# Optimization experiments

Hardware: AMD Instinct MI355X
Metric: run time of the kernel (lower is better)

The kernel has to match this reference:

```python
import jax, jax.numpy as jnp
import numpy as np

EMBED_DIM = 1024
KEY_SIZE = 1024
VALUE_SIZE = 1024


def setup_inputs() -> dict:
    key = jax.random.key(0)
    k1, k2, k3, k4, k5 = jax.random.split(key, 5)
    B, L = 4, 4096
    s = 1.0 / np.sqrt(EMBED_DIM)
    return {
        "x": jax.random.normal(k1, (B, L, EMBED_DIM), dtype=jnp.float32),
        # torch nn.Linear weights: [out_features, in_features]
        "Wq": jax.random.normal(k2, (KEY_SIZE, EMBED_DIM), dtype=jnp.float32) * s,
        "Wk": jax.random.normal(k3, (KEY_SIZE, EMBED_DIM), dtype=jnp.float32) * s,
        "Wv": jax.random.normal(k4, (VALUE_SIZE, EMBED_DIM), dtype=jnp.float32) * s,
        "Wo": jax.random.normal(k5, (EMBED_DIM, VALUE_SIZE), dtype=jnp.float32) * s,
    }


def reference(x, Wq, Wk, Wv, Wo):
    # x: [B, L, E]
    q = jnp.einsum("ble,ke->blk", x, Wq)  # [B, L, K]
    k = jnp.einsum("ble,ke->blk", x, Wk)  # [B, L, K]
    v = jnp.einsum("ble,ve->blv", x, Wv)  # [B, L, V]
    K = k.shape[-1]
    # transposed (feature-axial) attention: att over feature dims, contracting seq L
    att = jnp.einsum("blk,blj->bkj", q, k) / jnp.sqrt(jnp.asarray(K, x.dtype))  # [B, K, K]
    att = jax.nn.softmax(att, axis=-1)
    # out[b,l,k] = sum_j att[b,k,j] * v[b,l,j]  (matmul(att, v^T) then transpose)
    out = jnp.einsum("bkj,blj->blk", att, v)  # [B, L, K]
    return jnp.einsum("blv,ev->ble", out, Wo)  # [B, L, E]
```

## Files before the change

### kernel.cpp

```cpp
#include <hip/hip_runtime.h>
#include <hip/hip_bf16.h>

typedef unsigned short u16;
typedef __bf16 bf16x8 __attribute__((ext_vector_type(8)));
typedef float f32x4 __attribute__((ext_vector_type(4)));
typedef unsigned short ushort8 __attribute__((ext_vector_type(8)));

#define AS1 __attribute__((address_space(1)))
#define AS3 __attribute__((address_space(3)))

__device__ inline u16 f2bf(float f) {
  union { float f; unsigned int u; } c; c.f = f;
  unsigned int u = c.u;
  return (u16)((u + 0x7fffu + ((u >> 16) & 1u)) >> 16);
}
__device__ inline float bf2f(u16 v) {
  union { unsigned int u; float f; } c; c.u = ((unsigned int)v) << 16;
  return c.f;
}

__global__ __launch_bounds__(256) void cvt_x_dual(const float* __restrict__ x,
                                                  u16* __restrict__ xbf,
                                                  u16* __restrict__ xT) {
  __shared__ u16 tile[64][68];
  const int t = threadIdx.x;
  const long e0 = (long)blockIdx.x * 64;
  const long l0 = (long)blockIdx.y * 64;
  const long b  = blockIdx.z;
  const int tr = t >> 4, tc = t & 15;
#pragma unroll
  for (int i = 0; i < 4; ++i) {
    const int r = tr + i * 16;
    const long gl = b * 4096 + l0 + r;
    float4 v = *reinterpret_cast<const float4*>(x + gl * 1024 + e0 + tc * 4);
    ushort4 o;
    o.x = f2bf(v.x); o.y = f2bf(v.y); o.z = f2bf(v.z); o.w = f2bf(v.w);
    *reinterpret_cast<ushort4*>(xbf + gl * 1024 + e0 + tc * 4) = o;
    *reinterpret_cast<ushort4*>(&tile[r][tc * 4]) = o;
  }
  __syncthreads();
#pragma unroll
  for (int i = 0; i < 4; ++i) {
    const int c = tr + i * 16;
    ushort4 o;
    o.x = tile[tc * 4 + 0][c]; o.y = tile[tc * 4 + 1][c];
    o.z = tile[tc * 4 + 2][c]; o.w = tile[tc * 4 + 3][c];
    *reinterpret_cast<ushort4*>(xT + b * (1024L * 4096) + (e0 + c) * 4096 + l0 + tc * 4) = o;
  }
}

__global__ __launch_bounds__(256) void cvt_w4(const float* __restrict__ a, const float* __restrict__ b,
                                              const float* __restrict__ c, const float* __restrict__ d,
                                              u16* __restrict__ oa, u16* __restrict__ ob,
                                              u16* __restrict__ oc, u16* __restrict__ od) {
  int i = blockIdx.x * 256 + threadIdx.x;
  const int which = i >> 18;
  const int j = i & 262143;
  const float* src = which == 0 ? a : which == 1 ? b : which == 2 ? c : d;
  u16* dst = which == 0 ? oa : which == 1 ? ob : which == 2 ? oc : od;
  float4 v = reinterpret_cast<const float4*>(src)[j];
  ushort4 o;
  o.x = f2bf(v.x); o.y = f2bf(v.y); o.z = f2bf(v.z); o.w = f2bf(v.w);
  reinterpret_cast<ushort4*>(dst)[j] = o;
}

__global__ __launch_bounds__(256) void transpose_bf16(
    const u16* __restrict__ src, long sLd, long sZ,
    u16* __restrict__ dst, long dLd, long dZ) {
  __shared__ u16 tile[64][68];
  const int t = threadIdx.x;
  const long r0 = (long)blockIdx.y * 64;
  const long c0 = (long)blockIdx.x * 64;
  const long z = blockIdx.z;
  const int tr = t >> 4, tc = t & 15;
#pragma unroll
  for (int i = 0; i < 4; ++i) {
    const int r = tr + i * 16;
    ushort4 v = *reinterpret_cast<const ushort4*>(src + z * sZ + (r0 + r) * sLd + c0 + tc * 4);
    *reinterpret_cast<ushort4*>(&tile[r][tc * 4]) = v;
  }
  __syncthreads();
#pragma unroll
  for (int i = 0; i < 4; ++i) {
    const int c = tr + i * 16;
    ushort4 o;
    o.x = tile[tc * 4 + 0][c]; o.y = tile[tc * 4 + 1][c];
    o.z = tile[tc * 4 + 2][c]; o.w = tile[tc * 4 + 3][c];
    *reinterpret_cast<ushort4*>(dst + z * dZ + (c0 + c) * dLd + r0 + tc * 4) = o;
  }
}

__device__ __forceinline__ void stage_half(const u16* __restrict__ g, long ld, int k0,
                                           u16* dst, int t) {
#pragma unroll
  for (int i = 0; i < 2; ++i) {
    const int c = i * 512 + t;
    const int r = c >> 3;
    const int s = c & 7;
    const int col = ((s ^ (r & 7)) << 3) + k0;
    __builtin_amdgcn_global_load_lds((const AS1 void*)(g + (long)r * ld + col),
                                     (AS3 void*)(dst + c * 8), 16, 0, 0);
  }
}

template<int N16>
__device__ __forceinline__ void stage_rows256(const u16* __restrict__ g, long ld, int k0,
                                              u16* dst, int t) {
#pragma unroll
  for (int i = 0; i < N16; ++i) {
    const int c = i * 256 + t;
    const int r = c >> 3;
    const int s = c & 7;
    const int col = ((s ^ (r & 7)) << 3) + k0;
    __builtin_amdgcn_global_load_lds((const AS1 void*)(g + (long)r * ld + col),
                                     (AS3 void*)(dst + c * 8), 16, 0, 0);
  }
}

__device__ __forceinline__ bf16x8 frag_ld(const u16* s, int row, int colb) {
  return *reinterpret_cast<const bf16x8*>(
      reinterpret_cast<const char*>(s) + row * 128 + (colb ^ ((row & 7) << 4)));
}

#define XCD_DECODE2(TM, TN)                                                  \
  const int nxy = gridDim.x * gridDim.y;                                     \
  int flat = blockIdx.x + gridDim.x * blockIdx.y + nxy * blockIdx.z;         \
  const int total = nxy * gridDim.z;                                         \
  const int qq = total >> 3;                                                 \
  flat = (flat & 7) * qq + (flat >> 3);                                      \
  const int z = flat / nxy;                                                  \
  const int wg = flat % nxy;                                                 \
  const long m0 = (long)(wg % gridDim.x) * (TM);                             \
  const long n0 = (long)(wg / gridDim.x) * (TN);

#define BAR_PRE()       do { asm volatile("s_waitcnt vmcnt(6)" ::: "memory"); \
                             __builtin_amdgcn_s_barrier(); \
                             asm volatile("" ::: "memory"); } while (0)
#define BAR_POST()      do { asm volatile("" ::: "memory"); \
                             __builtin_amdgcn_s_barrier(); \
                             asm volatile("" ::: "memory"); } while (0)

template<bool OUT_F32>
__global__ __launch_bounds__(512, 2) void gemm_nt256(
    const u16* __restrict__ A, long lda, long sAz4, long sAz1,
    const u16* __restrict__ B, long ldb, long sBz4, long sBz1,
    void* __restrict__ Cv, long ldc, long sCz4, long sCz1,
    long cBatch, int cShift,
    int K, float scale)
{
  __shared__ u16 sm[2 * 32768] __attribute__((aligned(16)));

  const int t = threadIdx.x;
  XCD_DECODE2(256, 256);
  const long azoff = (long)(z >> 2) * sAz4 + (long)(z & 3) * sAz1;
  const long bzoff = (long)(z >> 2) * sBz4 + (long)(z & 3) * sBz1;
  const u16* Ab = A + azoff + m0 * lda;
  const u16* Bb = B + bzoff + n0 * ldb;

  const int wid = t >> 6, lane = t & 63;
  const int lhi = lane >> 4, llo = lane & 15;
  const int wm = wid >> 2, wn = wid & 3;

  f32x4 acc[2][4][2][2] = {};
  const int NT = K >> 6;

  stage_half(Ab, lda, 0, sm, t);
  stage_half(Bb + 128 * ldb, ldb, 0, sm + 16384 + 8192, t);
  stage_half(Bb, ldb, 0, sm + 16384, t);
  stage_half(Ab + 128 * lda, lda, 0, sm + 8192, t);
  stage_half(Ab, lda, 64, sm + 32768, t);
  stage_half(Bb + 128 * ldb, ldb, 64, sm + 32768 + 16384 + 8192, t);
  asm volatile("s_waitcnt vmcnt(4)" ::: "memory");
  __builtin_amdgcn_s_barrier();
  asm volatile("" ::: "memory");

  for (int kt = 0; kt < NT; ++kt) {
    const int kb = kt & 1;
    u16* bc = sm + kb * 32768;
    u16* bn = sm + (kb ^ 1) * 32768;
    const u16* sAc = bc;
    const u16* sBc = bc + 16384;
    const int k1 = ((kt + 1 < NT) ? kt + 1 : 0) << 6;
    const int k2 = ((kt + 2 < NT) ? kt + 2 : kt + 2 - NT) << 6;

    bf16x8 a[4][2], bl[2][2], bh[2][2];

#pragma unroll
    for (int fr = 0; fr < 4; ++fr)
#pragma unroll
      for (int kk = 0; kk < 2; ++kk)
        a[fr][kk] = frag_ld(sAc, wm * 64 + fr * 16 + llo, (kk << 6) + (lhi << 4));
#pragma unroll
    for (int fc = 0; fc < 2; ++fc)
#pragma unroll
      for (int kk = 0; kk < 2; ++kk)
        bl[fc][kk] = frag_ld(sBc, wn * 32 + fc * 16 + llo, (kk << 6) + (lhi << 4));
    stage_half(Bb, ldb, k1, bn + 16384, t);
    BAR_PRE();
    __builtin_amdgcn_s_setprio(1);
#pragma unroll
    for (int fr = 0; fr < 4; ++fr)
#pragma unroll
      for (int fc = 0; fc < 2; ++fc)
#pragma unroll
        for (int kk = 0; kk < 2; ++kk)
          acc[0][fr][0][fc] = __builtin_amdgcn_mfma_f32_16x16x32_bf16(a[fr][kk], bl[fc][kk], acc[0][fr][0][fc], 0, 0, 0);
    __builtin_amdgcn_s_setprio(0);
    BAR_POST();

#pragma unroll
    for (int fc = 0; fc < 2; ++fc)
#pragma unroll
      for (int kk = 0; kk < 2; ++kk)
        bh[fc][kk] = frag_ld(sBc, 128 + wn * 32 + fc * 16 + llo, (kk << 6) + (lhi << 4));
    stage_half(Ab + 128 * lda, lda, k1, bn + 8192, t);
    BAR_PRE();
    __builtin_amdgcn_s_setprio(1);
#pragma unroll
    for (int fr = 0; fr < 4; ++fr)
#pragma unroll
      for (int fc = 0; fc < 2; ++fc)
#pragma unroll
        for (int kk = 0; kk < 2; ++kk)
          acc[0][fr][1][fc] = __builtin_amdgcn_mfma_f32_16x16x32_bf16(a[fr][kk], bh[fc][kk], acc[0][fr][1][fc], 0, 0, 0);
    __builtin_amdgcn_s_setprio(0);
    BAR_POST();

#pragma unroll
    for (int fr = 0; fr < 4; ++fr)
#pragma unroll
      for (int kk = 0; kk < 2; ++kk)
        a[fr][kk] = frag_ld(sAc, 128 + wm * 64 + fr * 16 + llo, (kk << 6) + (lhi << 4));
    stage_half(Ab, lda, k2, bc, t);
    BAR_PRE();
    __builtin_amdgcn_s_setprio(1);
#pragma unroll
    for (int fr = 0; fr < 4; ++fr)
#pragma unroll
      for (int fc = 0; fc < 2; ++fc)
#pragma unroll
        for (int kk = 0; kk < 2; ++kk)
          acc[1][fr][1][fc] = __builtin_amdgcn_mfma_f32_16x16x32_bf16(a[fr][kk], bh[fc][kk], acc[1][fr][1][fc], 0, 0, 0);
    __builtin_amdgcn_s_setprio(0);
    BAR_POST();

    stage_half(Bb + 128 * ldb, ldb, k2, bc + 16384 + 8192, t);
    BAR_PRE();
    __builtin_amdgcn_s_setprio(1);
#pragma unroll
    for (int fr = 0; fr < 4; ++fr)
#pragma unroll
      for (int fc = 0; fc < 2; ++fc)
#pragma unroll
        for (int kk = 0; kk < 2; ++kk)
          acc[1][fr][0][fc] = __builtin_amdgcn_mfma_f32_16x16x32_bf16(a[fr][kk], bl[fc][kk], acc[1][fr][0][fc], 0, 0, 0);
    __builtin_amdgcn_s_setprio(0);
    BAR_POST();
  }

  const long cb = n0 >> cShift;
  const long ncol0 = n0 - (cb << cShift);
  const long czoff = (long)(z >> 2) * sCz4 + (long)(z & 3) * sCz1 + cb * cBatch;
#pragma unroll
  for (int ah = 0; ah < 2; ++ah)
#pragma unroll
    for (int fr = 0; fr < 4; ++fr)
#pragma unroll
      for (int e = 0; e < 4; ++e) {
        const long r = m0 + ah * 128 + wm * 64 + fr * 16 + lhi * 4 + e;
#pragma unroll
        for (int bh2 = 0; bh2 < 2; ++bh2)
#pragma unroll
          for (int fc = 0; fc < 2; ++fc) {
            const long col = ncol0 + bh2 * 128 + wn * 32 + fc * 16 + llo;
            const float val = acc[ah][fr][bh2][fc][e] * scale;
            if (OUT_F32)
              ((float*)Cv)[czoff + r * ldc + col] = val;
            else
              ((u16*)Cv)[czoff + r * ldc + col] = f2bf(val);
          }
      }
}

template<bool OUT_F32>
__global__ __launch_bounds__(256, 3) void gemm_nt128x64(
    const u16* __restrict__ A, long lda, long sAz,
    const u16* __restrict__ B, long ldb, long sBz,
    void* __restrict__ Cv, long ldc, long sCz,
    int K, float scale)
{
  __shared__ u16 sm[2 * 12288] __attribute__((aligned(16)));

  const int t = threadIdx.x;
  XCD_DECODE2(128, 64);
  A += (long)z * sAz + m0 * lda;
  B += (long)z * sBz + n0 * ldb;

  const int wid = t >> 6, lane = t & 63;
  const int lhi = lane >> 4, llo = lane & 15;
  const int wr = (wid >> 1) * 64, wc = (wid & 1) * 32;

  f32x4 acc[4][2] = {};
  const int NT = K >> 6;

  stage_rows256<4>(A, lda, 0, sm, t);
  stage_rows256<2>(B, ldb, 0, sm + 8192, t);
  stage_rows256<4>(A, lda, 64, sm + 12288, t);
  stage_rows256<2>(B, ldb, 64, sm + 12288 + 8192, t);

  for (int kt = 0; kt < NT; ++kt) {
    asm volatile("s_waitcnt vmcnt(6)" ::: "memory");
    __builtin_amdgcn_s_barrier();
    asm volatile("" ::: "memory");
    u16* buf = sm + (kt & 1) * 12288;
    bf16x8 af[4][2], bfr[2][2];
#pragma unroll
    for (int i = 0; i < 4; ++i)
#pragma unroll
      for (int kk = 0; kk < 2; ++kk)
        af[i][kk] = frag_ld(buf, wr + i * 16 + llo, (kk << 6) + (lhi << 4));
#pragma unroll
    for (int j = 0; j < 2; ++j)
#pragma unroll
      for (int kk = 0; kk < 2; ++kk)
        bfr[j][kk] = frag_ld(buf + 8192, wc + j * 16 + llo, (kk << 6) + (lhi << 4));
    __builtin_amdgcn_s_setprio(1);
#pragma unroll
    for (int i = 0; i < 4; ++i)
#pragma unroll
      for (int j = 0; j < 2; ++j)
#pragma unroll
        for (int kk = 0; kk < 2; ++kk)
          acc[i][j] = __builtin_amdgcn_mfma_f32_16x16x32_bf16(af[i][kk], bfr[j][kk], acc[i][j], 0, 0, 0);
    __builtin_amdgcn_s_setprio(0);
    asm volatile("" ::: "memory");
    __builtin_amdgcn_s_barrier();
    asm volatile("" ::: "memory");
    const int k2 = ((kt + 2 < NT) ? kt + 2 : kt + 2 - NT) << 6;
    stage_rows256<4>(A, lda, k2, buf, t);
    stage_rows256<2>(B, ldb, k2, buf + 8192, t);
  }

#pragma unroll
  for (int i = 0; i < 4; ++i) {
#pragma unroll
    for (int e = 0; e < 4; ++e) {
      const long r = m0 + wr + i * 16 + lhi * 4 + e;
      if (OUT_F32) {
        float* C = (float*)Cv + (long)z * sCz + r * ldc + n0 + wc + llo;
#pragma unroll
        for (int j = 0; j < 2; ++j) C[j * 16] = acc[i][j][e] * scale;
      } else {
        u16* C = (u16*)Cv + (long)z * sCz + r * ldc + n0 + wc + llo;
#pragma unroll
        for (int j = 0; j < 2; ++j) C[j * 16] = f2bf(acc[i][j][e] * scale);
      }
    }
  }
}

__global__ __launch_bounds__(256) void greduce4b(const u16* __restrict__ gp,
                                                 u16* __restrict__ gb) {
  const long o = (long)blockIdx.x * 256 + threadIdx.x;
  const long b = o >> 17;
  const long r = o & 131071;
  float s[8] = {};
#pragma unroll
  for (int p = 0; p < 4; ++p) {
    ushort8 u = reinterpret_cast<const ushort8*>(gp)[((b * 4 + p) << 17) + r];
#pragma unroll
    for (int j = 0; j < 8; ++j) s[j] += bf2f(u[j]);
  }
  ushort8 out;
#pragma unroll
  for (int j = 0; j < 8; ++j) out[j] = f2bf(s[j]);
  reinterpret_cast<ushort8*>(gb)[o] = out;
}

__global__ __launch_bounds__(256) void softmax1(const float* __restrict__ att,
                                                u16* __restrict__ P) {
  const long row = blockIdx.x;
  const int t = threadIdx.x;
  float4 v = reinterpret_cast<const float4*>(att + row * 1024)[t];
  float m = fmaxf(fmaxf(v.x, v.y), fmaxf(v.z, v.w));
#pragma unroll
  for (int off = 32; off > 0; off >>= 1) m = fmaxf(m, __shfl_down(m, off, 64));
  __shared__ float smax[4], ssum[4];
  const int wid = t >> 6, lane = t & 63;
  if (lane == 0) smax[wid] = m;
  __syncthreads();
  m = fmaxf(fmaxf(smax[0], smax[1]), fmaxf(smax[2], smax[3]));
  float e0 = expf(v.x - m), e1 = expf(v.y - m), e2 = expf(v.z - m), e3 = expf(v.w - m);
  float s = e0 + e1 + e2 + e3;
#pragma unroll
  for (int off = 32; off > 0; off >>= 1) s += __shfl_down(s, off, 64);
  if (lane == 0) ssum[wid] = s;
  __syncthreads();
  s = ssum[0] + ssum[1] + ssum[2] + ssum[3];
  float inv = 1.0f / s;
  ushort4 o;
  o.x = f2bf(e0 * inv); o.y = f2bf(e1 * inv); o.z = f2bf(e2 * inv); o.w = f2bf(e3 * inv);
  reinterpret_cast<ushort4*>(P + row * 1024)[t] = o;
}

extern "C" void kernel_launch(void* const* d_in, const int* in_sizes, int n_in,
                              void* d_out, int out_size, void* d_ws, size_t ws_size,
                              hipStream_t stream) {
  const float* x  = (const float*)d_in[0];
  const float* Wq = (const float*)d_in[1];
  const float* Wk = (const float*)d_in[2];
  const float* Wv = (const float*)d_in[3];
  const float* Wo = (const float*)d_in[4];

  const long M1 = 1L << 20;

  u16* xbf    = (u16*)d_ws;
  u16* wq     = xbf + 16 * M1;
  u16* wk     = wq + M1;
  u16* wv     = wk + M1;
  u16* wo     = wv + M1;
  u16* wvT    = wo + M1;
  u16* xT     = wvT + M1;
  u16* gbf    = xT + 16 * M1;
  u16* tbuf   = gbf + 4 * M1;
  u16* pbuf   = tbuf + 4 * M1;
  u16* rtb    = pbuf + 4 * M1;
  u16* sbuf   = rtb + 4 * M1;
  u16* gpartb = sbuf + 4 * M1;
  float* attf = (float*)d_out;

  dim3 b256(256), b512(512);
  const long NOF = 0;
  const int NSH = 30;

  cvt_x_dual<<<dim3(16, 64, 4), b256, 0, stream>>>(x, xbf, xT);
  cvt_w4<<<dim3(4096), b256, 0, stream>>>(Wq, Wk, Wv, Wo, wq, wk, wv, wo);
  transpose_bf16<<<dim3(16, 16, 1), b256, 0, stream>>>(wv, 1024, 0, wvT, 1024, 0);

  gemm_nt256<false><<<dim3(4, 4, 16), b512, 0, stream>>>(
      xT, 4096, 1024L * 4096, 1024, xT, 4096, 1024L * 4096, 1024,
      (void*)gpartb, 1024, 4L << 20, 1L << 20, NOF, NSH, 1024, 1.0f);
  greduce4b<<<dim3(2048), b256, 0, stream>>>(gpartb, gbf);

  gemm_nt128x64<false><<<dim3(8, 16, 4), b256, 0, stream>>>(
      wq, 1024, 0, gbf, 1024, M1, (void*)tbuf, 1024, M1, 1024, 1.0f);
  gemm_nt128x64<true><<<dim3(8, 16, 4), b256, 0, stream>>>(
      tbuf, 1024, M1, wk, 1024, 0, (void*)attf, 1024, M1, 1024, 1.0f / 32.0f);
  softmax1<<<dim3(4096), b256, 0, stream>>>(attf, pbuf);

  gemm_nt128x64<false><<<dim3(8, 16, 4), b256, 0, stream>>>(
      wvT, 1024, 0, pbuf, 1024, M1, (void*)rtb, 1024, M1, 1024, 1.0f);
  gemm_nt128x64<false><<<dim3(8, 16, 4), b256, 0, stream>>>(
      wo, 1024, 0, rtb, 1024, M1, (void*)sbuf, 1024, M1, 1024, 1.0f);

  gemm_nt256<true><<<dim3(16, 4, 4), b512, 0, stream>>>(
      xbf, 1024, 0, 4096L * 1024, sbuf, 1024, 0, M1,
      d_out, 1024, 0, 4096L * 1024, NOF, NSH, 1024, 1.0f);
}
```

Before: 185.7 us.

## Unroll 256x256 GEMM main loop by two with reordered half-tile prefetch schedule

Restructures the 256x256 bf16 GEMM main loop into a two-k-tile unrolled body with fixed buffer pointers and a reordered sequence of global-to-LDS half-tile stages (three halves of the next tile prefetched up front instead of two). Barriers now explicitly wait on lgkmcnt(0) after the barrier and use sched_barrier to pin the schedule, with a partial lgkmcnt hint after fragment reads; the vmcnt wait moves to only the last phase of each tile. The aim is to cut per-iteration index arithmetic and spread vmem waits so MFMA phases overlap loads better, at the risk of subtle ordering hazards and an implicit assumption that NT is even.

```diff
diff --git a/kernel.cpp b/kernel.cpp
--- a/kernel.cpp
+++ b/kernel.cpp
@@ -122,6 +122,32 @@
       reinterpret_cast<const char*>(s) + row * 128 + (colb ^ ((row & 7) << 4)));
 }
 
+__device__ __forceinline__ void read_a(bf16x8 (&a)[4][2], const u16* half, int wrow, int llo, int lhi) {
+#pragma unroll
+  for (int fr = 0; fr < 4; ++fr)
+#pragma unroll
+    for (int kk = 0; kk < 2; ++kk)
+      a[fr][kk] = frag_ld(half, wrow + fr * 16 + llo, (kk << 6) + (lhi << 4));
+}
+__device__ __forceinline__ void read_b(bf16x8 (&b)[2][2], const u16* half, int wcol, int llo, int lhi) {
+#pragma unroll
+  for (int fc = 0; fc < 2; ++fc)
+#pragma unroll
+    for (int kk = 0; kk < 2; ++kk)
+      b[fc][kk] = frag_ld(half, wcol + fc * 16 + llo, (kk << 6) + (lhi << 4));
+}
+__device__ __forceinline__ void mfma_quad(f32x4 (&q)[4][2], bf16x8 (&af)[4][2], bf16x8 (&bf)[2][2]) {
+  __builtin_amdgcn_s_setprio(1);
+#pragma unroll
+  for (int fr = 0; fr < 4; ++fr)
+#pragma unroll
+    for (int fc = 0; fc < 2; ++fc)
+#pragma unroll
+      for (int kk = 0; kk < 2; ++kk)
+        q[fr][fc] = __builtin_amdgcn_mfma_f32_16x16x32_bf16(af[fr][kk], bf[fc][kk], q[fr][fc], 0, 0, 0);
+  __builtin_amdgcn_s_setprio(0);
+}
+
 #define XCD_DECODE2(TM, TN)                                                  \
   const int nxy = gridDim.x * gridDim.y;                                     \
   int flat = blockIdx.x + gridDim.x * blockIdx.y + nxy * blockIdx.z;         \
@@ -133,12 +159,17 @@
   const long m0 = (long)(wg % gridDim.x) * (TM);                             \
   const long n0 = (long)(wg / gridDim.x) * (TN);
 
-#define BAR_PRE()       do { asm volatile("s_waitcnt vmcnt(6)" ::: "memory"); \
-                             __builtin_amdgcn_s_barrier(); \
-                             asm volatile("" ::: "memory"); } while (0)
-#define BAR_POST()      do { asm volatile("" ::: "memory"); \
-                             __builtin_amdgcn_s_barrier(); \
-                             asm volatile("" ::: "memory"); } while (0)
+#define PH_SYNC()    do { __builtin_amdgcn_s_barrier();                           \
+                          asm volatile("s_waitcnt lgkmcnt(0)" ::: "memory");      \
+                          __builtin_amdgcn_sched_barrier(0); } while (0)
+#define PH_SYNC_VM() do { asm volatile("s_waitcnt vmcnt(6)" ::: "memory");        \
+                          __builtin_amdgcn_s_barrier();                           \
+                          asm volatile("s_waitcnt lgkmcnt(0)" ::: "memory");      \
+                          __builtin_amdgcn_sched_barrier(0); } while (0)
+#define PH_END()     do { asm volatile("" ::: "memory");                          \
+                          __builtin_amdgcn_s_barrier();                           \
+                          asm volatile("" ::: "memory"); } while (0)
+#define LGKM_HINT()  asm volatile("s_waitcnt lgkmcnt(8)" ::: "memory")
 
 template<bool OUT_F32>
 __global__ __launch_bounds__(512, 2) void gemm_nt256(
@@ -160,102 +191,81 @@
   const int wid = t >> 6, lane = t & 63;
   const int lhi = lane >> 4, llo = lane & 15;
   const int wm = wid >> 2, wn = wid & 3;
-
-  f32x4 acc[2][4][2][2] = {};
+  const int war = wm * 64;
+  const int wbc = wn * 32;
+
+  u16* buf0 = sm;
+  u16* buf1 = sm + 32768;
+  f32x4 acc[2][2][4][2] = {};
   const int NT = K >> 6;
 
-  stage_half(Ab, lda, 0, sm, t);
-  stage_half(Bb + 128 * ldb, ldb, 0, sm + 16384 + 8192, t);
-  stage_half(Bb, ldb, 0, sm + 16384, t);
-  stage_half(Ab + 128 * lda, lda, 0, sm + 8192, t);
-  stage_half(Ab, lda, 64, sm + 32768, t);
-  stage_half(Bb + 128 * ldb, ldb, 64, sm + 32768 + 16384 + 8192, t);
-  asm volatile("s_waitcnt vmcnt(4)" ::: "memory");
+  stage_half(Ab, lda, 0, buf0, t);
+  stage_half(Bb, ldb, 0, buf0 + 16384, t);
+  stage_half(Bb + 128 * ldb, ldb, 0, buf0 + 24576, t);
+  stage_half(Ab + 128 * lda, lda, 0, buf0 + 8192, t);
+  stage_half(Ab, lda, 64, buf1, t);
+  stage_half(Bb, ldb, 64, buf1 + 16384, t);
+  stage_half(Bb + 128 * ldb, ldb, 64, buf1 + 24576, t);
+  asm volatile("s_waitcnt vmcnt(6)" ::: "memory");
   __builtin_amdgcn_s_barrier();
   asm volatile("" ::: "memory");
 
-  for (int kt = 0; kt < NT; ++kt) {
-    const int kb = kt & 1;
-    u16* bc = sm + kb * 32768;
-    u16* bn = sm + (kb ^ 1) * 32768;
-    const u16* sAc = bc;
-    const u16* sBc = bc + 16384;
-    const int k1 = ((kt + 1 < NT) ? kt + 1 : 0) << 6;
-    const int k2 = ((kt + 2 < NT) ? kt + 2 : kt + 2 - NT) << 6;
-
-    bf16x8 a[4][2], bl[2][2], bh[2][2];
-
-#pragma unroll
-    for (int fr = 0; fr < 4; ++fr)
-#pragma unroll
-      for (int kk = 0; kk < 2; ++kk)
-        a[fr][kk] = frag_ld(sAc, wm * 64 + fr * 16 + llo, (kk << 6) + (lhi << 4));
-#pragma unroll
-    for (int fc = 0; fc < 2; ++fc)
-#pragma unroll
-      for (int kk = 0; kk < 2; ++kk)
-        bl[fc][kk] = frag_ld(sBc, wn * 32 + fc * 16 + llo, (kk << 6) + (lhi << 4));
-    stage_half(Bb, ldb, k1, bn + 16384, t);
-    BAR_PRE();
-    __builtin_amdgcn_s_setprio(1);
-#pragma unroll
-    for (int fr = 0; fr < 4; ++fr)
-#pragma unroll
-      for (int fc = 0; fc < 2; ++fc)
-#pragma unroll
-        for (int kk = 0; kk < 2; ++kk)
-          acc[0][fr][0][fc] = __builtin_amdgcn_mfma_f32_16x16x32_bf16(a[fr][kk], bl[fc][kk], acc[0][fr][0][fc], 0, 0, 0);
-    __builtin_amdgcn_s_setprio(0);
-    BAR_POST();
-
-#pragma unroll
-    for (int fc = 0; fc < 2; ++fc)
-#pragma unroll
-      for (int kk = 0; kk < 2; ++kk)
-        bh[fc][kk] = frag_ld(sBc, 128 + wn * 32 + fc * 16 + llo, (kk << 6) + (lhi << 4));
-    stage_half(Ab + 128 * lda, lda, k1, bn + 8192, t);
-    BAR_PRE();
-    __builtin_amdgcn_s_setprio(1);
-#pragma unroll
-    for (int fr = 0; fr < 4; ++fr)
-#pragma unroll
-      for (int fc = 0; fc < 2; ++fc)
-#pragma unroll
-        for (int kk = 0; kk < 2; ++kk)
-          acc[0][fr][1][fc] = __builtin_amdgcn_mfma_f32_16x16x32_bf16(a[fr][kk], bh[fc][kk], acc[0][fr][1][fc], 0, 0, 0);
-    __builtin_amdgcn_s_setprio(0);
-    BAR_POST();
-
-#pragma unroll
-    for (int fr = 0; fr < 4; ++fr)
-#pragma unroll
-      for (int kk = 0; kk < 2; ++kk)
-        a[fr][kk] = frag_ld(sAc, 128 + wm * 64 + fr * 16 + llo, (kk << 6) + (lhi << 4));
-    stage_half(Ab, lda, k2, bc, t);
-    BAR_PRE();
-    __builtin_amdgcn_s_setprio(1);
-#pragma unroll
-    for (int fr = 0; fr < 4; ++fr)
-#pragma unroll
-      for (int fc = 0; fc < 2; ++fc)
-#pragma unroll
-        for (int kk = 0; kk < 2; ++kk)
-          acc[1][fr][1][fc] = __builtin_amdgcn_mfma_f32_16x16x32_bf16(a[fr][kk], bh[fc][kk], acc[1][fr][1][fc], 0, 0, 0);
-    __builtin_amdgcn_s_setprio(0);
-    BAR_POST();
-
-    stage_half(Bb + 128 * ldb, ldb, k2, bc + 16384 + 8192, t);
-    BAR_PRE();
-    __builtin_amdgcn_s_setprio(1);
-#pragma unroll
-    for (int fr = 0; fr < 4; ++fr)
-#pragma unroll
-      for (int fc = 0; fc < 2; ++fc)
-#pragma unroll
-        for (int kk = 0; kk < 2; ++kk)
-          acc[1][fr][0][fc] = __builtin_amdgcn_mfma_f32_16x16x32_bf16(a[fr][kk], bl[fc][kk], acc[1][fr][0][fc], 0, 0, 0);
-    __builtin_amdgcn_s_setprio(0);
-    BAR_POST();
+  for (int it = 0; it < (NT >> 1); ++it) {
+    const int k1b = (2 * it + 1) << 6;
+    const int t2a = 2 * it + 2, t2b = 2 * it + 3;
+    const int k2a = ((t2a < NT) ? t2a : t2a - NT) << 6;
+    const int k2b = ((t2b < NT) ? t2b : t2b - NT) << 6;
+    bf16x8 aLo[4][2], aHi[4][2], bLo[2][2], bHi[2][2];
+
+    read_a(aLo, buf0, war, llo, lhi);
+    read_b(bLo, buf0 + 16384, wbc, llo, lhi);
+    stage_half(Ab + 128 * lda, lda, k1b, buf1 + 8192, t);
+    LGKM_HINT();
+    PH_SYNC();
+    mfma_quad(acc[0][0], aLo, bLo);
+    PH_END();
+
+    read_b(bHi, buf0 + 24576, wbc, llo, lhi);
+    stage_half(Ab, lda, k2a, buf0, t);
+    PH_SYNC();
+    mfma_quad(acc[0][1], aLo, bHi);
+    PH_END();
+
+    read_a(aHi, buf0 + 8192, war, llo, lhi);
+    stage_half(Bb, ldb, k2a, buf0 + 16384, t);
+    PH_SYNC();
+    mfma_quad(acc[1][1], aHi, bHi);
+    PH_END();
+
+    stage_half(Bb + 128 * ldb, ldb, k2a, buf0 + 24576, t);
+    PH_SYNC_VM();
+    mfma_quad(acc[1][0], aHi, bLo);
+    PH_END();
+
+    read_a(aLo, buf1, war, llo, lhi);
+    read_b(bLo, buf1 + 16384, wbc, llo, lhi);
+    stage_half(Ab + 128 * lda, lda, k2a, buf0 + 8192, t);
+    LGKM_HINT();
+    PH_SYNC();
+    mfma_quad(acc[0][0], aLo, bLo);
+    PH_END();
+
+    read_b(bHi, buf1 + 24576, wbc, llo, lhi);
+    stage_half(Ab, lda, k2b, buf1, t);
+    PH_SYNC();
+    mfma_quad(acc[0][1], aLo, bHi);
+    PH_END();
+
+    read_a(aHi, buf1 + 8192, war, llo, lhi);
+    stage_half(Bb, ldb, k2b, buf1 + 16384, t);
+    PH_SYNC();
+    mfma_quad(acc[1][1], aHi, bHi);
+    PH_END();
+
+    stage_half(Bb + 128 * ldb, ldb, k2b, buf1 + 24576, t);
+    PH_SYNC_VM();
+    mfma_quad(acc[1][0], aHi, bLo);
+    PH_END();
   }
 
   const long cb = n0 >> cShift;
@@ -273,7 +283,7 @@
 #pragma unroll
           for (int fc = 0; fc < 2; ++fc) {
             const long col = ncol0 + bh2 * 128 + wn * 32 + fc * 16 + llo;
-            const float val = acc[ah][fr][bh2][fc][e] * scale;
+            const float val = acc[ah][bh2][fr][fc][e] * scale;
             if (OUT_F32)
               ((float*)Cv)[czoff + r * ldc + col] = val;
             else
```

Measured after the change: 190.6 us. 1.03x slower.
